# Optimization experiments

Hardware: AMD Instinct MI355X
Metric: run time of the kernel (lower is better)

The kernel has to match this reference:

```python
import jax, jax.numpy as jnp
import numpy as np

B, S, D_IN, D_CODE, K = 8, 4096, 1024, 64, 4096


def setup_inputs() -> dict:
    key = jax.random.key(0)
    k1, k2, k3, k4 = jax.random.split(key, 4)
    return {
        "input": jax.random.normal(k1, (B, S, D_IN), dtype=jnp.float32),
        "W_send": jax.random.normal(k2, (D_IN, D_CODE), dtype=jnp.float32) * (1.0 / np.sqrt(D_IN)),
        "b_send": jnp.zeros((D_CODE,), dtype=jnp.float32),
        "emb": jax.random.normal(k3, (K, D_CODE), dtype=jnp.float32),
        "W_recv": jax.random.normal(k4, (D_CODE, D_IN), dtype=jnp.float32) * (1.0 / np.sqrt(D_CODE)),
        "b_recv": jnp.zeros((D_IN,), dtype=jnp.float32),
    }


def reference(input, W_send, b_send, emb, W_recv, b_recv):
    # encoder: z = send(input) -> [B, S, D_CODE]
    z = jnp.einsum('bsi,ic->bsc', input, W_send) + b_send

    # VQEmbedding.lookup: argmin_k ||e_k||^2 - 2 <z, e_k>  (no-grad path)
    sqr = jnp.sum(emb * emb, axis=1)                      # [K]
    cov = jnp.einsum('bsc,kc->bsk', z, emb)               # [B, S, K]
    indices = jnp.argmin(sqr - 2.0 * cov, axis=-1)        # [B, S] int

    # fetch embeddings (gather)
    vectors = emb[indices]                                # [B, S, D_CODE]

    # straight-through estimator: values = z + sg(vectors - z)
    values = z + jax.lax.stop_gradient(vectors - z)

    # decoder: x = recv(values) -> [B, S, D_IN]
    x = jnp.einsum('bsc,ci->bsi', values, W_recv) + b_recv

    # VQEmbedding.loss (reduction='sum')
    embedding_loss = jnp.sum((vectors - jax.lax.stop_gradient(z)) ** 2)
    commitment_loss = jnp.sum((z - jax.lax.stop_gradient(vectors)) ** 2)

    # empirical code entropy in bits
    num_codes = emb.shape[0]
    counts = jnp.bincount(indices.ravel(), length=num_codes)
    p = counts.astype(jnp.float32) / jnp.float32(indices.size)
    ent = -jnp.sum(jnp.where(p > 0, p * jnp.log(jnp.where(p > 0, p, 1.0)), 0.0)) / jnp.log(2.0)

    return x, indices, embedding_loss, commitment_loss, ent
```

## Files before the change

### kernel.cpp

```cpp
#include <hip/hip_runtime.h>

#define DIN 1024
#define DC 64
#define KC 4096

typedef _Float16 f16x8 __attribute__((ext_vector_type(8)));
typedef _Float16 f16x4 __attribute__((ext_vector_type(4)));
typedef float f32x4 __attribute__((ext_vector_type(4)));

__device__ __forceinline__ void gll16(const void* g, void* l) {
    __builtin_amdgcn_global_load_lds(
        (const __attribute__((address_space(1))) unsigned int*)g,
        (__attribute__((address_space(3))) unsigned int*)l, 16, 0, 0);
}

__global__ __launch_bounds__(256) void k_prep(const float* __restrict__ emb,
                                              const float* __restrict__ Ws,
                                              const float* __restrict__ Wr,
                                              const float* __restrict__ br,
                                              _Float16* __restrict__ Ee,
                                              float* __restrict__ sqr,
                                              _Float16* __restrict__ Wh,
                                              float* __restrict__ D,
                                              int* __restrict__ counts) {
    int b = blockIdx.x;
    int tid = threadIdx.x;
    if (b < 1024) {
        int code = b * 4 + (tid >> 6);
        int lane = tid & 63;
        float v = emb[(size_t)code * DC + lane];
        Ee[(size_t)code * 64 + lane] = (_Float16)v;
        float s = v * v;
        #pragma unroll
        for (int m = 1; m < 64; m <<= 1) s += __shfl_xor(s, m);
        if (lane == 0) sqr[code] = s;
        if (tid < 4) counts[b * 4 + tid] = 0;
        return;
    }
    if (b < 1040) {
        int k0 = (b - 1024) * 64;
        #pragma unroll
        for (int it = 0; it < 16; ++it) {
            int q = it * 256 + tid;
            int c = q >> 6, kl = q & 63;
            float v = Ws[(size_t)(k0 + kl) * 64 + c];
            Wh[(size_t)c * 1024 + k0 + kl] = (_Float16)v;
        }
        return;
    }
    __shared__ float Ek[64][68];
    __shared__ float Wt[64][132];
    int bb = b - 1040;
    int cb0  = (bb & 63) * 64;
    int col0 = (bb >> 6) * 128;
    int tx = tid & 15;
    int ty = tid >> 4;

    for (int q = tid; q < 1024; q += 256) {
        int r = q >> 4, c4 = q & 15;
        float4 v = *(const float4*)&emb[(size_t)(cb0 + r) * DC + c4*4];
        Ek[c4*4+0][r] = v.x; Ek[c4*4+1][r] = v.y;
        Ek[c4*4+2][r] = v.z; Ek[c4*4+3][r] = v.w;
    }
    for (int q = tid; q < 2048; q += 256) {
        int c = q >> 5, k4 = q & 31;
        *(float4*)&Wt[c][k4*4] = *(const float4*)&Wr[(size_t)c * DIN + col0 + k4*4];
    }
    __syncthreads();

    float acc[4][8] = {};
    #pragma unroll 8
    for (int c = 0; c < 64; ++c) {
        float4 av = *(const float4*)&Ek[c][tx*4];
        float4 w0 = *(const float4*)&Wt[c][ty*8];
        float4 w1 = *(const float4*)&Wt[c][ty*8 + 4];
        float a[4] = {av.x, av.y, av.z, av.w};
        float w[8] = {w0.x, w0.y, w0.z, w0.w, w1.x, w1.y, w1.z, w1.w};
        #pragma unroll
        for (int i = 0; i < 4; ++i)
            #pragma unroll
            for (int j = 0; j < 8; ++j)
                acc[i][j] += a[i] * w[j];
    }

    #pragma unroll
    for (int i = 0; i < 4; ++i) {
        int code = cb0 + tx*4 + i;
        float4 o0, o1;
        o0.x = acc[i][0] + br[col0 + ty*8 + 0];
        o0.y = acc[i][1] + br[col0 + ty*8 + 1];
        o0.z = acc[i][2] + br[col0 + ty*8 + 2];
        o0.w = acc[i][3] + br[col0 + ty*8 + 3];
        o1.x = acc[i][4] + br[col0 + ty*8 + 4];
        o1.y = acc[i][5] + br[col0 + ty*8 + 5];
        o1.z = acc[i][6] + br[col0 + ty*8 + 6];
        o1.w = acc[i][7] + br[col0 + ty*8 + 7];
        *(float4*)&D[(size_t)code * DIN + col0 + ty*8]     = o0;
        *(float4*)&D[(size_t)code * DIN + col0 + ty*8 + 4] = o1;
    }
}

__global__ __launch_bounds__(256) void k_send(const float* __restrict__ in,
                                              const _Float16* __restrict__ Wh,
                                              const float* __restrict__ bs,
                                              _Float16* __restrict__ Ze) {
    __shared__ char smem[32768];
    const int tid = threadIdx.x;
    const int row0 = blockIdx.x * 64;
    const int wid = tid >> 6, lane = tid & 63;
    const int c15 = lane & 15, g = lane >> 4;
    const int wm = wid >> 1, wn = wid & 1;

    f32x4 acc[2][2];
    const f32x4 z4 = {0.f, 0.f, 0.f, 0.f};
    #pragma unroll
    for (int mf = 0; mf < 2; ++mf)
        #pragma unroll
        for (int nf = 0; nf < 2; ++nf) acc[mf][nf] = z4;

    int abyte[2], aswz[2], bbyte[2], bswz[2];
    #pragma unroll
    for (int mf = 0; mf < 2; ++mf) {
        int r = wm * 32 + mf * 16 + c15;
        abyte[mf] = r * 128; aswz[mf] = (r & 7) << 4;
    }
    #pragma unroll
    for (int nf = 0; nf < 2; ++nf) {
        int c = wn * 32 + nf * 16 + c15;
        bbyte[nf] = c * 128; bswz[nf] = (c & 7) << 4;
    }
    const int g16 = g * 16;

    auto stageB = [&](int buf, int s) {
        char* dst = smem + buf * 16384 + 8192;
        #pragma unroll
        for (int r = 0; r < 2; ++r) {
            int p = r * 4096 + wid * 1024 + lane * 16;
            int row = p >> 7, off = p & 127;
            int soff = off ^ ((row & 7) << 4);
            gll16((const char*)Wh + (size_t)row * 2048 + s * 128 + soff,
                  dst + p);
        }
    };

    auto loadA = [&](int s, float4* a) {
        #pragma unroll
        for (int it = 0; it < 4; ++it) {
            int q = it * 256 + tid;
            int r = q >> 4, c4 = q & 15;
            a[it] = *(const float4*)&in[(size_t)(row0 + r) * DIN + s * 64 + c4 * 4];
        }
    };

    auto writeA = [&](int buf, const float4* a) {
        char* Ah = smem + buf * 16384;
        #pragma unroll
        for (int it = 0; it < 4; ++it) {
            int q = it * 256 + tid;
            int r = q >> 4, c4 = q & 15;
            float v[4] = {a[it].x, a[it].y, a[it].z, a[it].w};
            f16x4 h;
            #pragma unroll
            for (int j = 0; j < 4; ++j) h[j] = (_Float16)v[j];
            int o = r * 128 + ((c4 * 8) ^ ((r & 7) << 4));
            *(f16x4*)(Ah + o) = h;
        }
    };

    auto compute = [&](int buf) {
        const char* Ah = smem + buf * 16384;
        const char* Bh = Ah + 8192;
        #pragma unroll
        for (int ks = 0; ks < 2; ++ks) {
            int koff = ks * 64 + g16;
            f16x8 bh[2];
            #pragma unroll
            for (int nf = 0; nf < 2; ++nf)
                bh[nf] = *(const f16x8*)(Bh + bbyte[nf] + (koff ^ bswz[nf]));
            #pragma unroll
            for (int mf = 0; mf < 2; ++mf) {
                f16x8 ah = *(const f16x8*)(Ah + abyte[mf] + (koff ^ aswz[mf]));
                #pragma unroll
                for (int nf = 0; nf < 2; ++nf)
                    acc[mf][nf] = __builtin_amdgcn_mfma_f32_16x16x32_f16(
                        ah, bh[nf], acc[mf][nf], 0, 0, 0);
            }
        }
    };

    {
        float4 a0[4];
        loadA(0, a0);
        stageB(0, 0);
        writeA(0, a0);
    }
    __syncthreads();

    for (int s = 0; s < 16; ++s) {
        int c = s & 1;
        float4 an[4];
        if (s < 15) {
            loadA(s + 1, an);
            stageB(c ^ 1, s + 1);
        }
        compute(c);
        if (s < 15) writeA(c ^ 1, an);
        __syncthreads();
    }

    #pragma unroll
    for (int nf = 0; nf < 2; ++nf) {
        int col = wn * 32 + nf * 16 + c15;
        float bias = bs[col];
        #pragma unroll
        for (int mf = 0; mf < 2; ++mf) {
            #pragma unroll
            for (int r2 = 0; r2 < 4; ++r2) {
                float zv = acc[mf][nf][r2] + bias;
                int row = row0 + wm * 32 + mf * 16 + g * 4 + r2;
                Ze[(size_t)row * 64 + col] = (_Float16)zv;
            }
        }
    }
}

__global__ __launch_bounds__(512, 4) void k_score(const _Float16* __restrict__ Ee,
                                                  const _Float16* __restrict__ Ze,
                                                  const float* __restrict__ sqr,
                                                  int* __restrict__ idx,
                                                  float* __restrict__ out_idx,
                                                  int* __restrict__ counts,
                                                  float* __restrict__ lpart) {
    __shared__ char smem[35072];
    const int tid = threadIdx.x;
    const int row0 = blockIdx.x * 64;
    const int wid = tid >> 6, lane = tid & 63;
    const int c15 = lane & 15, g = lane >> 4;
    const int wm = wid >> 1;
    const int wn = wid & 1;
    const int g16 = g * 16;

    f16x8 zfh[2][2];
    #pragma unroll
    for (int nf = 0; nf < 2; ++nf) {
        const _Float16* zr = Ze + (size_t)(row0 + wn * 32 + nf * 16 + c15) * 64;
        #pragma unroll
        for (int j = 0; j < 2; ++j)
            zfh[j][nf] = *(const f16x8*)(zr + j * 32 + g * 8);
    }

    int rbase[2], rx[2];
    #pragma unroll
    for (int mf = 0; mf < 2; ++mf) {
        int r = wm * 32 + mf * 16 + c15;
        rbase[mf] = r * 128;
        rx[mf] = (r & 7) << 4;
    }

    auto stage = [&](int ch, int buf) {
        char* dst = smem + buf * 16384;
        const char* src = (const char*)Ee + (size_t)ch * 16384;
        #pragma unroll
        for (int t = 0; t < 2; ++t) {
            int p = t * 8192 + tid * 16;
            int r = p >> 7, b = p & 127;
            gll16(src + r * 128 + (b ^ ((r & 7) << 4)), dst + p);
        }
    };

    float bv[2];
    int   bi[2];
    #pragma unroll
    for (int nf = 0; nf < 2; ++nf) { bv[nf] = 3.402823466e38f; bi[nf] = 0; }

    const f32x4 zz4 = {0.f, 0.f, 0.f, 0.f};

    stage(0, 0);
    __syncthreads();

    for (int ch = 0; ch < 32; ++ch) {
        const int buf = ch & 1;
        f32x4 sqv[2];
        #pragma unroll
        for (int mf = 0; mf < 2; ++mf)
            sqv[mf] = *(const f32x4*)(sqr + ch * 128 + wm * 32 + mf * 16 + g * 4);

        if (ch < 31) stage(ch + 1, buf ^ 1);

        const char* base = smem + buf * 16384;
        f32x4 acc[2][2];
        #pragma unroll
        for (int j = 0; j < 2; ++j) {
            const int kbyte = j * 64 + g16;
            f16x8 af[2];
            #pragma unroll
            for (int mf = 0; mf < 2; ++mf)
                af[mf] = *(const f16x8*)(base + rbase[mf] + (kbyte ^ rx[mf]));
            #pragma unroll
            for (int mf = 0; mf < 2; ++mf)
                #pragma unroll
                for (int nf = 0; nf < 2; ++nf)
                    acc[mf][nf] = __builtin_amdgcn_mfma_f32_16x16x32_f16(
                        af[mf], zfh[j][nf],
                        j == 0 ? zz4 : acc[mf][nf], 0, 0, 0);
        }

        #pragma unroll
        for (int nf = 0; nf < 2; ++nf) {
            #pragma unroll
            for (int mf = 0; mf < 2; ++mf) {
                f32x4 v = sqv[mf] - acc[mf][nf] * 2.0f;
                #pragma unroll
                for (int r2 = 0; r2 < 4; ++r2) {
                    if (v[r2] < bv[nf]) {
                        bv[nf] = v[r2];
                        bi[nf] = ch * 128 + wm * 32 + mf * 16 + g * 4 + r2;
                    }
                }
            }
        }
        __syncthreads();
    }

    float* redv = (float*)(smem + 32768);
    int*   redi = (int*)(smem + 33792);
    float* zsqa = (float*)(smem + 34816);

    #pragma unroll
    for (int nf = 0; nf < 2; ++nf) {
        float v_ = bv[nf]; int i_ = bi[nf];
        #pragma unroll
        for (int m = 16; m <= 32; m <<= 1) {
            float ov = __shfl_xor(v_, m);
            int oi = __shfl_xor(i_, m);
            if (ov < v_ || (ov == v_ && oi < i_)) { v_ = ov; i_ = oi; }
        }
        if (g == 0) {
            int rl = wn * 32 + nf * 16 + c15;
            redv[wm * 64 + rl] = v_;
            redi[wm * 64 + rl] = i_;
        }
    }
    if (wm == 0) {
        #pragma unroll
        for (int nf = 0; nf < 2; ++nf) {
            float s = 0.f;
            #pragma unroll
            for (int j = 0; j < 2; ++j)
                #pragma unroll
                for (int e = 0; e < 8; ++e) {
                    float zv = (float)zfh[j][nf][e];
                    s += zv * zv;
                }
            s += __shfl_xor(s, 16);
            s += __shfl_xor(s, 32);
            if (g == 0) zsqa[wn * 32 + nf * 16 + c15] = s;
        }
    }
    __syncthreads();
    if (tid < 64) {
        float v0 = redv[tid]; int i0 = redi[tid];
        #pragma unroll
        for (int w = 1; w < 4; ++w) {
            float v1 = redv[w * 64 + tid]; int i1 = redi[w * 64 + tid];
            if (v1 < v0 || (v1 == v0 && i1 < i0)) { v0 = v1; i0 = i1; }
        }
        int grow = row0 + tid;
        idx[grow] = i0;
        out_idx[grow] = (float)i0;
        atomicAdd(&counts[i0], 1);
        float lossv = v0 + zsqa[tid];
        #pragma unroll
        for (int m = 1; m < 64; m <<= 1) lossv += __shfl_xor(lossv, m);
        if (tid == 0) lpart[blockIdx.x] = lossv;
    }
}

__global__ __launch_bounds__(256) void k_gather(const float* __restrict__ D,
                                                const int* __restrict__ idx,
                                                const int* __restrict__ counts,
                                                const float* __restrict__ lpart,
                                                float* __restrict__ x,
                                                float* __restrict__ out_sc) {
    int tid = threadIdx.x;
    if (blockIdx.x == 2048) {
        __shared__ float red[256];
        red[tid] = lpart[tid] + lpart[256 + tid];
        __syncthreads();
        for (int s = 128; s > 0; s >>= 1) {
            if (tid < s) red[tid] += red[tid + s];
            __syncthreads();
        }
        float loss = red[0];
        __syncthreads();
        float ep = 0.f;
        for (int k = tid; k < KC; k += 256) {
            int c = counts[k];
            if (c > 0) {
                float p = (float)c / 32768.0f;
                ep += p * logf(p);
            }
        }
        red[tid] = ep; __syncthreads();
        for (int s = 128; s > 0; s >>= 1) {
            if (tid < s) red[tid] += red[tid + s];
            __syncthreads();
        }
        if (tid == 0) {
            out_sc[0] = loss;
            out_sc[1] = loss;
            out_sc[2] = -red[0] * 1.4426950408889634f;
        }
        return;
    }
    int gidx = blockIdx.x * 256 + tid;
    #pragma unroll
    for (int it = 0; it < 4; ++it) {
        int f = gidx + it * 524288;
        int row = f >> 6, c = f & 63;
        int code = idx[row];
        *(float4*)&x[(size_t)row * DIN + c*4] =
            *(const float4*)&D[(size_t)code * DIN + c*4];
    }
}

extern "C" void kernel_launch(void* const* d_in, const int* in_sizes, int n_in,
                              void* d_out, int out_size, void* d_ws, size_t ws_size,
                              hipStream_t stream) {
    (void)in_sizes; (void)n_in; (void)out_size; (void)ws_size;
    const float* input  = (const float*)d_in[0];
    const float* W_send = (const float*)d_in[1];
    const float* b_send = (const float*)d_in[2];
    const float* emb    = (const float*)d_in[3];
    const float* W_recv = (const float*)d_in[4];
    const float* b_recv = (const float*)d_in[5];
    float* out = (float*)d_out;

    char* ws = (char*)d_ws;
    _Float16* Ze  = (_Float16*)(ws);
    float*    D   = (float*)(ws + 4194304);
    _Float16* Ee  = (_Float16*)(ws + 20971520);
    float*    sqr = (float*)(ws + 21495808);
    int*      idx = (int*)  (ws + 21512192);
    int*   counts = (int*)  (ws + 21643264);
    float* lpart  = (float*)(ws + 21659648);
    _Float16* Wh  = (_Float16*)(ws + 21661696);

    float* out_x   = out;
    float* out_idx = out + 33554432;
    float* out_sc  = out + 33587200;

    k_prep<<<1552, 256, 0, stream>>>(emb, W_send, W_recv, b_recv,
                                     Ee, sqr, Wh, D, counts);
    k_send<<<512, 256, 0, stream>>>(input, Wh, b_send, Ze);
    k_score<<<512, 512, 0, stream>>>(Ee, Ze, sqr, idx, out_idx, counts, lpart);
    k_gather<<<2049, 256, 0, stream>>>(D, idx, counts, lpart, out_x, out_sc);
}
```

Baseline: 86.82 us.

## Fuse encoder with code scoring and compute decoder output via fp16 MFMA

Merges the send GEMM and codebook scoring into one kernel, keeping z in shared memory instead of writing it to and reading it back from global memory. It also drops the precomputed fp32 table of emb@W_recv (16MB) and instead computes each output row with an MFMA GEMM of the gathered fp16 codes against a transposed fp16 W_recv. This removes the large prep GEMM and the 16MB table traffic. The cost is fp16 rounding in the decoder and a score loop with 256 threads instead of 512, which gives less parallelism per block.

```diff
diff --git a/kernel.cpp b/kernel.cpp
--- a/kernel.cpp
+++ b/kernel.cpp
@@ -17,11 +17,10 @@
 __global__ __launch_bounds__(256) void k_prep(const float* __restrict__ emb,
                                               const float* __restrict__ Ws,
                                               const float* __restrict__ Wr,
-                                              const float* __restrict__ br,
                                               _Float16* __restrict__ Ee,
                                               float* __restrict__ sqr,
                                               _Float16* __restrict__ Wh,
-                                              float* __restrict__ D,
+                                              _Float16* __restrict__ WrT,
                                               int* __restrict__ counts) {
     int b = blockIdx.x;
     int tid = threadIdx.x;
@@ -48,75 +47,38 @@
         }
         return;
     }
-    __shared__ float Ek[64][68];
-    __shared__ float Wt[64][132];
-    int bb = b - 1040;
-    int cb0  = (bb & 63) * 64;
-    int col0 = (bb >> 6) * 128;
-    int tx = tid & 15;
-    int ty = tid >> 4;
-
-    for (int q = tid; q < 1024; q += 256) {
-        int r = q >> 4, c4 = q & 15;
-        float4 v = *(const float4*)&emb[(size_t)(cb0 + r) * DC + c4*4];
-        Ek[c4*4+0][r] = v.x; Ek[c4*4+1][r] = v.y;
-        Ek[c4*4+2][r] = v.z; Ek[c4*4+3][r] = v.w;
-    }
-    for (int q = tid; q < 2048; q += 256) {
-        int c = q >> 5, k4 = q & 31;
-        *(float4*)&Wt[c][k4*4] = *(const float4*)&Wr[(size_t)c * DIN + col0 + k4*4];
-    }
-    __syncthreads();
-
-    float acc[4][8] = {};
-    #pragma unroll 8
-    for (int c = 0; c < 64; ++c) {
-        float4 av = *(const float4*)&Ek[c][tx*4];
-        float4 w0 = *(const float4*)&Wt[c][ty*8];
-        float4 w1 = *(const float4*)&Wt[c][ty*8 + 4];
-        float a[4] = {av.x, av.y, av.z, av.w};
-        float w[8] = {w0.x, w0.y, w0.z, w0.w, w1.x, w1.y, w1.z, w1.w};
-        #pragma unroll
-        for (int i = 0; i < 4; ++i)
-            #pragma unroll
-            for (int j = 0; j < 8; ++j)
-                acc[i][j] += a[i] * w[j];
-    }
-
-    #pragma unroll
-    for (int i = 0; i < 4; ++i) {
-        int code = cb0 + tx*4 + i;
-        float4 o0, o1;
-        o0.x = acc[i][0] + br[col0 + ty*8 + 0];
-        o0.y = acc[i][1] + br[col0 + ty*8 + 1];
-        o0.z = acc[i][2] + br[col0 + ty*8 + 2];
-        o0.w = acc[i][3] + br[col0 + ty*8 + 3];
-        o1.x = acc[i][4] + br[col0 + ty*8 + 4];
-        o1.y = acc[i][5] + br[col0 + ty*8 + 5];
-        o1.z = acc[i][6] + br[col0 + ty*8 + 6];
-        o1.w = acc[i][7] + br[col0 + ty*8 + 7];
-        *(float4*)&D[(size_t)code * DIN + col0 + ty*8]     = o0;
-        *(float4*)&D[(size_t)code * DIN + col0 + ty*8 + 4] = o1;
+    int b2 = b - 1040;
+    #pragma unroll
+    for (int it = 0; it < 16; ++it) {
+        int k = it * 4 + (tid >> 6);
+        int rr = b2 * 64 + (tid & 63);
+        WrT[(size_t)rr * 64 + k] = (_Float16)Wr[(size_t)k * 1024 + rr];
     }
 }
 
-__global__ __launch_bounds__(256) void k_send(const float* __restrict__ in,
+__global__ __launch_bounds__(256) void k_main(const float* __restrict__ in,
                                               const _Float16* __restrict__ Wh,
                                               const float* __restrict__ bs,
-                                              _Float16* __restrict__ Ze) {
+                                              const _Float16* __restrict__ Ee,
+                                              const float* __restrict__ sqr,
+                                              int* __restrict__ idx,
+                                              float* __restrict__ out_idx,
+                                              int* __restrict__ counts,
+                                              float* __restrict__ lpart) {
     __shared__ char smem[32768];
     const int tid = threadIdx.x;
     const int row0 = blockIdx.x * 64;
     const int wid = tid >> 6, lane = tid & 63;
     const int c15 = lane & 15, g = lane >> 4;
+    const int g16 = g * 16;
     const int wm = wid >> 1, wn = wid & 1;
 
     f32x4 acc[2][2];
-    const f32x4 z4 = {0.f, 0.f, 0.f, 0.f};
+    const f32x4 zz4 = {0.f, 0.f, 0.f, 0.f};
     #pragma unroll
     for (int mf = 0; mf < 2; ++mf)
         #pragma unroll
-        for (int nf = 0; nf < 2; ++nf) acc[mf][nf] = z4;
+        for (int nf = 0; nf < 2; ++nf) acc[mf][nf] = zz4;
 
     int abyte[2], aswz[2], bbyte[2], bswz[2];
     #pragma unroll
@@ -129,7 +91,6 @@
         int c = wn * 32 + nf * 16 + c15;
         bbyte[nf] = c * 128; bswz[nf] = (c & 7) << 4;
     }
-    const int g16 = g * 16;
 
     auto stageB = [&](int buf, int s) {
         char* dst = smem + buf * 16384 + 8192;
@@ -142,7 +103,6 @@
                   dst + p);
         }
     };
-
     auto loadA = [&](int s, float4* a) {
         #pragma unroll
         for (int it = 0; it < 4; ++it) {
@@ -151,7 +111,6 @@
             a[it] = *(const float4*)&in[(size_t)(row0 + r) * DIN + s * 64 + c4 * 4];
         }
     };
-
     auto writeA = [&](int buf, const float4* a) {
         char* Ah = smem + buf * 16384;
         #pragma unroll
@@ -166,7 +125,6 @@
             *(f16x4*)(Ah + o) = h;
         }
     };
-
     auto compute = [&](int buf) {
         const char* Ah = smem + buf * 16384;
         const char* Bh = Ah + 8192;
@@ -195,7 +153,6 @@
         writeA(0, a0);
     }
     __syncthreads();
-
     for (int s = 0; s < 16; ++s) {
         int c = s & 1;
         float4 an[4];
@@ -208,63 +165,49 @@
         __syncthreads();
     }
 
+    char* Zt = smem + 16384;
     #pragma unroll
     for (int nf = 0; nf < 2; ++nf) {
-        int col = wn * 32 + nf * 16 + c15;
-        float bias = bs[col];
-        #pragma unroll
-        for (int mf = 0; mf < 2; ++mf) {
+        int k = wn * 32 + nf * 16 + c15;
+        float bias = bs[k];
+        #pragma unroll
+        for (int mf = 0; mf < 2; ++mf)
             #pragma unroll
             for (int r2 = 0; r2 < 4; ++r2) {
-                float zv = acc[mf][nf][r2] + bias;
-                int row = row0 + wm * 32 + mf * 16 + g * 4 + r2;
-                Ze[(size_t)row * 64 + col] = (_Float16)zv;
+                int row = wm * 32 + mf * 16 + g * 4 + r2;
+                _Float16 zh = (_Float16)(acc[mf][nf][r2] + bias);
+                *(_Float16*)(Zt + row * 128 + ((k * 2) ^ ((row & 7) << 4))) = zh;
             }
-        }
-    }
-}
-
-__global__ __launch_bounds__(512, 4) void k_score(const _Float16* __restrict__ Ee,
-                                                  const _Float16* __restrict__ Ze,
-                                                  const float* __restrict__ sqr,
-                                                  int* __restrict__ idx,
-                                                  float* __restrict__ out_idx,
-                                                  int* __restrict__ counts,
-                                                  float* __restrict__ lpart) {
-    __shared__ char smem[35072];
-    const int tid = threadIdx.x;
-    const int row0 = blockIdx.x * 64;
-    const int wid = tid >> 6, lane = tid & 63;
-    const int c15 = lane & 15, g = lane >> 4;
-    const int wm = wid >> 1;
-    const int wn = wid & 1;
-    const int g16 = g * 16;
-
+    }
+    __syncthreads();
+
+    const int wm2 = wm, wn2 = wn;
     f16x8 zfh[2][2];
     #pragma unroll
     for (int nf = 0; nf < 2; ++nf) {
-        const _Float16* zr = Ze + (size_t)(row0 + wn * 32 + nf * 16 + c15) * 64;
+        int zr = wn2 * 32 + nf * 16 + c15;
+        int sw = (zr & 7) << 4;
         #pragma unroll
         for (int j = 0; j < 2; ++j)
-            zfh[j][nf] = *(const f16x8*)(zr + j * 32 + g * 8);
+            zfh[j][nf] = *(const f16x8*)(Zt + zr * 128 + ((j * 64 + g16) ^ sw));
     }
 
     int rbase[2], rx[2];
     #pragma unroll
     for (int mf = 0; mf < 2; ++mf) {
-        int r = wm * 32 + mf * 16 + c15;
+        int r = wm2 * 32 + mf * 16 + c15;
         rbase[mf] = r * 128;
         rx[mf] = (r & 7) << 4;
     }
 
-    auto stage = [&](int ch, int buf) {
-        char* dst = smem + buf * 16384;
-        const char* src = (const char*)Ee + (size_t)ch * 16384;
+    auto stageE = [&](int ch, int buf) {
+        char* dst = smem + buf * 8192;
+        const char* src = (const char*)Ee + (size_t)ch * 8192;
         #pragma unroll
         for (int t = 0; t < 2; ++t) {
-            int p = t * 8192 + tid * 16;
-            int r = p >> 7, b = p & 127;
-            gll16(src + r * 128 + (b ^ ((r & 7) << 4)), dst + p);
+            int p = t * 4096 + tid * 16;
+            int r = p >> 7, off = p & 127;
+            gll16(src + r * 128 + (off ^ ((r & 7) << 4)), dst + p);
         }
     };
 
@@ -273,22 +216,20 @@
     #pragma unroll
     for (int nf = 0; nf < 2; ++nf) { bv[nf] = 3.402823466e38f; bi[nf] = 0; }
 
-    const f32x4 zz4 = {0.f, 0.f, 0.f, 0.f};
-
-    stage(0, 0);
-    __syncthreads();
-
-    for (int ch = 0; ch < 32; ++ch) {
+    stageE(0, 0);
+    __syncthreads();
+
+    for (int ch = 0; ch < 64; ++ch) {
         const int buf = ch & 1;
         f32x4 sqv[2];
         #pragma unroll
         for (int mf = 0; mf < 2; ++mf)
-            sqv[mf] = *(const f32x4*)(sqr + ch * 128 + wm * 32 + mf * 16 + g * 4);
-
-        if (ch < 31) stage(ch + 1, buf ^ 1);
-
-        const char* base = smem + buf * 16384;
-        f32x4 acc[2][2];
+            sqv[mf] = *(const f32x4*)(sqr + ch * 64 + wm2 * 32 + mf * 16 + g * 4);
+
+        if (ch < 63) stageE(ch + 1, buf ^ 1);
+
+        const char* base = smem + buf * 8192;
+        f32x4 sacc[2][2];
         #pragma unroll
         for (int j = 0; j < 2; ++j) {
             const int kbyte = j * 64 + g16;
@@ -300,21 +241,21 @@
             for (int mf = 0; mf < 2; ++mf)
                 #pragma unroll
                 for (int nf = 0; nf < 2; ++nf)
-                    acc[mf][nf] = __builtin_amdgcn_mfma_f32_16x16x32_f16(
+                    sacc[mf][nf] = __builtin_amdgcn_mfma_f32_16x16x32_f16(
                         af[mf], zfh[j][nf],
-                        j == 0 ? zz4 : acc[mf][nf], 0, 0, 0);
+                        j == 0 ? zz4 : sacc[mf][nf], 0, 0, 0);
         }
 
         #pragma unroll
         for (int nf = 0; nf < 2; ++nf) {
             #pragma unroll
             for (int mf = 0; mf < 2; ++mf) {
-                f32x4 v = sqv[mf] - acc[mf][nf] * 2.0f;
+                f32x4 v = sqv[mf] - sacc[mf][nf] * 2.0f;
                 #pragma unroll
                 for (int r2 = 0; r2 < 4; ++r2) {
                     if (v[r2] < bv[nf]) {
                         bv[nf] = v[r2];
-                        bi[nf] = ch * 128 + wm * 32 + mf * 16 + g * 4 + r2;
+                        bi[nf] = ch * 64 + wm2 * 32 + mf * 16 + g * 4 + r2;
                     }
                 }
             }
@@ -322,9 +263,9 @@
         __syncthreads();
     }
 
-    float* redv = (float*)(smem + 32768);
-    int*   redi = (int*)(smem + 33792);
-    float* zsqa = (float*)(smem + 34816);
+    float* redv = (float*)(smem + 24576);
+    int*   redi = (int*)(smem + 25088);
+    float* zsqa = (float*)(smem + 25600);
 
     #pragma unroll
     for (int nf = 0; nf < 2; ++nf) {
@@ -336,12 +277,12 @@
             if (ov < v_ || (ov == v_ && oi < i_)) { v_ = ov; i_ = oi; }
         }
         if (g == 0) {
-            int rl = wn * 32 + nf * 16 + c15;
-            redv[wm * 64 + rl] = v_;
-            redi[wm * 64 + rl] = i_;
-        }
-    }
-    if (wm == 0) {
+            int rl = wn2 * 32 + nf * 16 + c15;
+            redv[wm2 * 64 + rl] = v_;
+            redi[wm2 * 64 + rl] = i_;
+        }
+    }
+    if (wm2 == 0) {
         #pragma unroll
         for (int nf = 0; nf < 2; ++nf) {
             float s = 0.f;
@@ -354,17 +295,14 @@
                 }
             s += __shfl_xor(s, 16);
             s += __shfl_xor(s, 32);
-            if (g == 0) zsqa[wn * 32 + nf * 16 + c15] = s;
+            if (g == 0) zsqa[wn2 * 32 + nf * 16 + c15] = s;
         }
     }
     __syncthreads();
     if (tid < 64) {
         float v0 = redv[tid]; int i0 = redi[tid];
-        #pragma unroll
-        for (int w = 1; w < 4; ++w) {
-            float v1 = redv[w * 64 + tid]; int i1 = redi[w * 64 + tid];
-            if (v1 < v0 || (v1 == v0 && i1 < i0)) { v0 = v1; i0 = i1; }
-        }
+        float v1 = redv[64 + tid]; int i1 = redi[64 + tid];
+        if (v1 < v0 || (v1 == v0 && i1 < i0)) { v0 = v1; i0 = i1; }
         int grow = row0 + tid;
         idx[grow] = i0;
         out_idx[grow] = (float)i0;
@@ -376,15 +314,19 @@
     }
 }
 
-__global__ __launch_bounds__(256) void k_gather(const float* __restrict__ D,
-                                                const int* __restrict__ idx,
-                                                const int* __restrict__ counts,
-                                                const float* __restrict__ lpart,
-                                                float* __restrict__ x,
-                                                float* __restrict__ out_sc) {
+__global__ __launch_bounds__(256) void k_recv(const _Float16* __restrict__ Ee,
+                                              const _Float16* __restrict__ WrT,
+                                              const float* __restrict__ br,
+                                              const int* __restrict__ idx,
+                                              const int* __restrict__ counts,
+                                              const float* __restrict__ lpart,
+                                              float* __restrict__ x,
+                                              float* __restrict__ out_sc) {
+    __shared__ char smem[24832];
     int tid = threadIdx.x;
-    if (blockIdx.x == 2048) {
-        __shared__ float red[256];
+
+    if (blockIdx.x == 512) {
+        float* red = (float*)smem;
         red[tid] = lpart[tid] + lpart[256 + tid];
         __syncthreads();
         for (int s = 128; s > 0; s >>= 1) {
@@ -413,14 +355,78 @@
         }
         return;
     }
-    int gidx = blockIdx.x * 256 + tid;
-    #pragma unroll
-    for (int it = 0; it < 4; ++it) {
-        int f = gidx + it * 524288;
-        int row = f >> 6, c = f & 63;
-        int code = idx[row];
-        *(float4*)&x[(size_t)row * DIN + c*4] =
-            *(const float4*)&D[(size_t)code * DIN + c*4];
+
+    const int row0 = blockIdx.x * 64;
+    const int wid = tid >> 6, lane = tid & 63;
+    const int c15 = lane & 15, g = lane >> 4;
+    const int g16 = g * 16;
+    int* sidx = (int*)(smem + 24576);
+
+    if (tid < 64) sidx[tid] = idx[row0 + tid];
+    __syncthreads();
+
+    #pragma unroll
+    for (int t = 0; t < 2; ++t) {
+        int p = t * 4096 + tid * 16;
+        int r = p >> 7, off = p & 127;
+        gll16((const char*)Ee + (size_t)sidx[r] * 128 + (off ^ ((r & 7) << 4)),
+              smem + p);
+    }
+
+    auto stageW = [&](int cc, int buf) {
+        char* dst = smem + 8192 + buf * 8192;
+        #pragma unroll
+        for (int t = 0; t < 2; ++t) {
+            int p = t * 4096 + tid * 16;
+            int r = p >> 7, off = p & 127;
+            gll16((const char*)WrT + (size_t)(cc * 64 + r) * 128
+                      + (off ^ ((r & 7) << 4)),
+                  dst + p);
+        }
+    };
+    stageW(0, 0);
+    __syncthreads();
+
+    int abase[4], ax[4];
+    #pragma unroll
+    for (int mf = 0; mf < 4; ++mf) {
+        int r = mf * 16 + c15;
+        abase[mf] = r * 128;
+        ax[mf] = (r & 7) << 4;
+    }
+    const int brow = wid * 16 + c15;
+    const int bbase = 8192 + brow * 128;
+    const int bx = (brow & 7) << 4;
+
+    const f32x4 zz4 = {0.f, 0.f, 0.f, 0.f};
+    for (int cc = 0; cc < 16; ++cc) {
+        const int buf = cc & 1;
+        if (cc < 15) stageW(cc + 1, buf ^ 1);
+
+        const int col = cc * 64 + wid * 16 + c15;
+        float bias = br[col];
+
+        f32x4 acc[4];
+        #pragma unroll
+        for (int j = 0; j < 2; ++j) {
+            const int kbyte = j * 64 + g16;
+            f16x8 bf = *(const f16x8*)(smem + buf * 8192 + bbase + (kbyte ^ bx));
+            #pragma unroll
+            for (int mf = 0; mf < 4; ++mf) {
+                f16x8 af = *(const f16x8*)(smem + abase[mf] + (kbyte ^ ax[mf]));
+                acc[mf] = __builtin_amdgcn_mfma_f32_16x16x32_f16(
+                    af, bf, j == 0 ? zz4 : acc[mf], 0, 0, 0);
+            }
+        }
+
+        #pragma unroll
+        for (int mf = 0; mf < 4; ++mf)
+            #pragma unroll
+            for (int r2 = 0; r2 < 4; ++r2)
+                x[(size_t)(row0 + mf * 16 + g * 4 + r2) * DIN + col]
+                    = acc[mf][r2] + bias;
+
+        __syncthreads();
     }
 }
 
@@ -437,22 +443,21 @@
     float* out = (float*)d_out;
 
     char* ws = (char*)d_ws;
-    _Float16* Ze  = (_Float16*)(ws);
-    float*    D   = (float*)(ws + 4194304);
-    _Float16* Ee  = (_Float16*)(ws + 20971520);
-    float*    sqr = (float*)(ws + 21495808);
-    int*      idx = (int*)  (ws + 21512192);
-    int*   counts = (int*)  (ws + 21643264);
-    float* lpart  = (float*)(ws + 21659648);
-    _Float16* Wh  = (_Float16*)(ws + 21661696);
+    _Float16* Ee  = (_Float16*)(ws);
+    float*    sqr = (float*)(ws + 524288);
+    int*      idx = (int*)  (ws + 540672);
+    int*   counts = (int*)  (ws + 671744);
+    float* lpart  = (float*)(ws + 688128);
+    _Float16* Wh  = (_Float16*)(ws + 690176);
+    _Float16* WrT = (_Float16*)(ws + 821248);
 
     float* out_x   = out;
     float* out_idx = out + 33554432;
     float* out_sc  = out + 33587200;
 
-    k_prep<<<1552, 256, 0, stream>>>(emb, W_send, W_recv, b_recv,
-                                     Ee, sqr, Wh, D, counts);
-    k_send<<<512, 256, 0, stream>>>(input, Wh, b_send, Ze);
-    k_score<<<512, 512, 0, stream>>>(Ee, Ze, sqr, idx, out_idx, counts, lpart);
-    k_gather<<<2049, 256, 0, stream>>>(D, idx, counts, lpart, out_x, out_sc);
+    k_prep<<<1056, 256, 0, stream>>>(emb, W_send, W_recv, Ee, sqr, Wh, WrT, counts);
+    k_main<<<512, 256, 0, stream>>>(input, Wh, b_send, Ee, sqr,
+                                    idx, out_idx, counts, lpart);
+    k_recv<<<513, 256, 0, stream>>>(Ee, WrT, b_recv, idx, counts, lpart,
+                                    out_x, out_sc);
 }
```

Measured after the change: 91.01 us. +4.8%, slower.

## Store decoded codebook table in fp16 and halve send-kernel row tile

Applied to the files above, without the earlier changes.

The precomputed decoded-codebook table D (code→output row) is now stored in fp16, which halves the table size and the gather kernel's read traffic; the gather widens fp16 back to fp32 when writing x. Separately, the encoder GEMM kernel now handles 32 rows per block instead of 64, doubling the grid to 1024 blocks for better occupancy and memory parallelism. The cost is that the x outputs carry fp16 rounding, and B tiles are staged twice as often across blocks.

```diff
diff --git a/kernel.cpp b/kernel.cpp
--- a/kernel.cpp
+++ b/kernel.cpp
@@ -21,7 +21,7 @@
                                               _Float16* __restrict__ Ee,
                                               float* __restrict__ sqr,
                                               _Float16* __restrict__ Wh,
-                                              float* __restrict__ D,
+                                              _Float16* __restrict__ Dh,
                                               int* __restrict__ counts) {
     int b = blockIdx.x;
     int tid = threadIdx.x;
@@ -86,17 +86,11 @@
     #pragma unroll
     for (int i = 0; i < 4; ++i) {
         int code = cb0 + tx*4 + i;
-        float4 o0, o1;
-        o0.x = acc[i][0] + br[col0 + ty*8 + 0];
-        o0.y = acc[i][1] + br[col0 + ty*8 + 1];
-        o0.z = acc[i][2] + br[col0 + ty*8 + 2];
-        o0.w = acc[i][3] + br[col0 + ty*8 + 3];
-        o1.x = acc[i][4] + br[col0 + ty*8 + 4];
-        o1.y = acc[i][5] + br[col0 + ty*8 + 5];
-        o1.z = acc[i][6] + br[col0 + ty*8 + 6];
-        o1.w = acc[i][7] + br[col0 + ty*8 + 7];
-        *(float4*)&D[(size_t)code * DIN + col0 + ty*8]     = o0;
-        *(float4*)&D[(size_t)code * DIN + col0 + ty*8 + 4] = o1;
+        f16x8 hv;
+        #pragma unroll
+        for (int j = 0; j < 8; ++j)
+            hv[j] = (_Float16)(acc[i][j] + br[col0 + ty*8 + j]);
+        *(f16x8*)&Dh[(size_t)code * DIN + col0 + ty*8] = hv;
     }
 }
 
@@ -104,35 +98,29 @@
                                               const _Float16* __restrict__ Wh,
                                               const float* __restrict__ bs,
                                               _Float16* __restrict__ Ze) {
-    __shared__ char smem[32768];
+    __shared__ char smem[24576];
     const int tid = threadIdx.x;
-    const int row0 = blockIdx.x * 64;
+    const int row0 = blockIdx.x * 32;
     const int wid = tid >> 6, lane = tid & 63;
     const int c15 = lane & 15, g = lane >> 4;
     const int wm = wid >> 1, wn = wid & 1;
-
-    f32x4 acc[2][2];
+    const int g16 = g * 16;
+
+    f32x4 acc[2];
     const f32x4 z4 = {0.f, 0.f, 0.f, 0.f};
-    #pragma unroll
-    for (int mf = 0; mf < 2; ++mf)
-        #pragma unroll
-        for (int nf = 0; nf < 2; ++nf) acc[mf][nf] = z4;
-
-    int abyte[2], aswz[2], bbyte[2], bswz[2];
-    #pragma unroll
-    for (int mf = 0; mf < 2; ++mf) {
-        int r = wm * 32 + mf * 16 + c15;
-        abyte[mf] = r * 128; aswz[mf] = (r & 7) << 4;
-    }
+    acc[0] = z4; acc[1] = z4;
+
+    int abyte, aswz;
+    { int r = wm * 16 + c15; abyte = r * 128; aswz = (r & 7) << 4; }
+    int bbyte[2], bswz[2];
     #pragma unroll
     for (int nf = 0; nf < 2; ++nf) {
         int c = wn * 32 + nf * 16 + c15;
         bbyte[nf] = c * 128; bswz[nf] = (c & 7) << 4;
     }
-    const int g16 = g * 16;
 
     auto stageB = [&](int buf, int s) {
-        char* dst = smem + buf * 16384 + 8192;
+        char* dst = smem + buf * 12288 + 4096;
         #pragma unroll
         for (int r = 0; r < 2; ++r) {
             int p = r * 4096 + wid * 1024 + lane * 16;
@@ -145,7 +133,7 @@
 
     auto loadA = [&](int s, float4* a) {
         #pragma unroll
-        for (int it = 0; it < 4; ++it) {
+        for (int it = 0; it < 2; ++it) {
             int q = it * 256 + tid;
             int r = q >> 4, c4 = q & 15;
             a[it] = *(const float4*)&in[(size_t)(row0 + r) * DIN + s * 64 + c4 * 4];
@@ -153,9 +141,9 @@
     };
 
     auto writeA = [&](int buf, const float4* a) {
-        char* Ah = smem + buf * 16384;
-        #pragma unroll
-        for (int it = 0; it < 4; ++it) {
+        char* Ah = smem + buf * 12288;
+        #pragma unroll
+        for (int it = 0; it < 2; ++it) {
             int q = it * 256 + tid;
             int r = q >> 4, c4 = q & 15;
             float v[4] = {a[it].x, a[it].y, a[it].z, a[it].w};
@@ -168,8 +156,8 @@
     };
 
     auto compute = [&](int buf) {
-        const char* Ah = smem + buf * 16384;
-        const char* Bh = Ah + 8192;
+        const char* Ah = smem + buf * 12288;
+        const char* Bh = Ah + 4096;
         #pragma unroll
         for (int ks = 0; ks < 2; ++ks) {
             int koff = ks * 64 + g16;
@@ -177,19 +165,16 @@
             #pragma unroll
             for (int nf = 0; nf < 2; ++nf)
                 bh[nf] = *(const f16x8*)(Bh + bbyte[nf] + (koff ^ bswz[nf]));
-            #pragma unroll
-            for (int mf = 0; mf < 2; ++mf) {
-                f16x8 ah = *(const f16x8*)(Ah + abyte[mf] + (koff ^ aswz[mf]));
-                #pragma unroll
-                for (int nf = 0; nf < 2; ++nf)
-                    acc[mf][nf] = __builtin_amdgcn_mfma_f32_16x16x32_f16(
-                        ah, bh[nf], acc[mf][nf], 0, 0, 0);
-            }
+            f16x8 ah = *(const f16x8*)(Ah + abyte + (koff ^ aswz));
+            #pragma unroll
+            for (int nf = 0; nf < 2; ++nf)
+                acc[nf] = __builtin_amdgcn_mfma_f32_16x16x32_f16(
+                    ah, bh[nf], acc[nf], 0, 0, 0);
         }
     };
 
     {
-        float4 a0[4];
+        float4 a0[2];
         loadA(0, a0);
         stageB(0, 0);
         writeA(0, a0);
@@ -198,7 +183,7 @@
 
     for (int s = 0; s < 16; ++s) {
         int c = s & 1;
-        float4 an[4];
+        float4 an[2];
         if (s < 15) {
             loadA(s + 1, an);
             stageB(c ^ 1, s + 1);
@@ -213,13 +198,9 @@
         int col = wn * 32 + nf * 16 + c15;
         float bias = bs[col];
         #pragma unroll
-        for (int mf = 0; mf < 2; ++mf) {
-            #pragma unroll
-            for (int r2 = 0; r2 < 4; ++r2) {
-                float zv = acc[mf][nf][r2] + bias;
-                int row = row0 + wm * 32 + mf * 16 + g * 4 + r2;
-                Ze[(size_t)row * 64 + col] = (_Float16)zv;
-            }
+        for (int r2 = 0; r2 < 4; ++r2) {
+            int row = row0 + wm * 16 + g * 4 + r2;
+            Ze[(size_t)row * 64 + col] = (_Float16)(acc[nf][r2] + bias);
         }
     }
 }
@@ -376,7 +357,7 @@
     }
 }
 
-__global__ __launch_bounds__(256) void k_gather(const float* __restrict__ D,
+__global__ __launch_bounds__(256) void k_gather(const _Float16* __restrict__ Dh,
                                                 const int* __restrict__ idx,
                                                 const int* __restrict__ counts,
                                                 const float* __restrict__ lpart,
@@ -415,12 +396,19 @@
     }
     int gidx = blockIdx.x * 256 + tid;
     #pragma unroll
-    for (int it = 0; it < 4; ++it) {
+    for (int it = 0; it < 8; ++it) {
         int f = gidx + it * 524288;
-        int row = f >> 6, c = f & 63;
+        int row = f >> 7, c8 = f & 127;
         int code = idx[row];
-        *(float4*)&x[(size_t)row * DIN + c*4] =
-            *(const float4*)&D[(size_t)code * DIN + c*4];
+        f16x8 v = *(const f16x8*)&Dh[(size_t)code * DIN + c8 * 8];
+        float4 o0, o1;
+        o0.x = (float)v[0]; o0.y = (float)v[1];
+        o0.z = (float)v[2]; o0.w = (float)v[3];
+        o1.x = (float)v[4]; o1.y = (float)v[5];
+        o1.z = (float)v[6]; o1.w = (float)v[7];
+        float* dst = &x[(size_t)row * DIN + c8 * 8];
+        *(float4*)dst = o0;
+        *(float4*)(dst + 4) = o1;
     }
 }
 
@@ -438,21 +426,21 @@
 
     char* ws = (char*)d_ws;
     _Float16* Ze  = (_Float16*)(ws);
-    float*    D   = (float*)(ws + 4194304);
-    _Float16* Ee  = (_Float16*)(ws + 20971520);
-    float*    sqr = (float*)(ws + 21495808);
-    int*      idx = (int*)  (ws + 21512192);
-    int*   counts = (int*)  (ws + 21643264);
-    float* lpart  = (float*)(ws + 21659648);
-    _Float16* Wh  = (_Float16*)(ws + 21661696);
+    _Float16* Dh  = (_Float16*)(ws + 4194304);
+    _Float16* Ee  = (_Float16*)(ws + 12582912);
+    float*    sqr = (float*)(ws + 13107200);
+    int*      idx = (int*)  (ws + 13123584);
+    int*   counts = (int*)  (ws + 13254656);
+    float* lpart  = (float*)(ws + 13271040);
+    _Float16* Wh  = (_Float16*)(ws + 13273088);
 
     float* out_x   = out;
     float* out_idx = out + 33554432;
     float* out_sc  = out + 33587200;
 
     k_prep<<<1552, 256, 0, stream>>>(emb, W_send, W_recv, b_recv,
-                                     Ee, sqr, Wh, D, counts);
-    k_send<<<512, 256, 0, stream>>>(input, Wh, b_send, Ze);
+                                     Ee, sqr, Wh, Dh, counts);
+    k_send<<<1024, 256, 0, stream>>>(input, Wh, b_send, Ze);
     k_score<<<512, 512, 0, stream>>>(Ee, Ze, sqr, idx, out_idx, counts, lpart);
-    k_gather<<<2049, 256, 0, stream>>>(D, idx, counts, lpart, out_x, out_sc);
-}
+    k_gather<<<2049, 256, 0, stream>>>(Dh, idx, counts, lpart, out_x, out_sc);
+}
```

Result: slower. 112.6 us (+29.7%).
